# Optimization experiments

Measured on AMD Instinct MI355X. Metric: run time of the kernel, lower is better.

Reference implementation:

```python
import jax, jax.numpy as jnp
import numpy as np

NUM_EMBEDDINGS = 8192
EMBEDDING_DIM = 512
COMMITMENT_COST = 0.25


def setup_inputs() -> dict:
    key = jax.random.key(0)
    kx, ke = jax.random.split(key)
    x = jax.random.normal(kx, (32, 512, 512), dtype=jnp.float32)
    # codebook ~ uniform init as in nn.Embedding default-ish; scale is arbitrary for a reference
    codebook = jax.random.normal(ke, (NUM_EMBEDDINGS, EMBEDDING_DIM), dtype=jnp.float32)
    return {"x": x, "codebook": codebook}


def reference(x, codebook):
    # x: [B, T, D], codebook: [K, D]
    input_shape = x.shape
    flat = x.reshape(-1, EMBEDDING_DIM)                     # [N, D]
    x2 = jnp.sum(flat * flat, axis=1, keepdims=True)        # [N, 1]
    e2 = jnp.sum(codebook * codebook, axis=1)               # [K]
    dists = x2 + e2 - 2.0 * jnp.matmul(flat, codebook.T)    # [N, K]
    encoding_indices = jnp.argmin(dists, axis=1)            # [N] int
    min_distances = jnp.min(dists, axis=1)                  # [N]
    quantized = codebook[encoding_indices].reshape(input_shape)  # [B, T, D]
    # straight-through estimator
    quantized_st = x + jax.lax.stop_gradient(quantized - x)
    # losses (sum reduction, matching F.mse_loss(..., reduction='sum'))
    loss_vq = jnp.sum((quantized - jax.lax.stop_gradient(x)) ** 2)
    loss_commit = jnp.sum((x - jax.lax.stop_gradient(quantized)) ** 2)
    # use_ema = False -> loss includes codebook term
    loss = loss_commit * COMMITMENT_COST + loss_vq
    encoding_indices = encoding_indices.reshape(input_shape[:-1])
    min_distances = min_distances.reshape(input_shape[:-1])
    return quantized_st, loss, encoding_indices, min_distances, loss_commit
```

## Files before the change

### kernel.cpp

```cpp
#include <hip/hip_runtime.h>
#include <hip/hip_bf16.h>
#include <math.h>

#define NUM_EMB 8192
#define DIM 512
#define NROWS 16384
#define NPART 4096

typedef unsigned short ushort;
typedef unsigned long long ull;
typedef __attribute__((ext_vector_type(8))) short short8;
typedef __attribute__((ext_vector_type(4))) float floatx4;

__device__ __forceinline__ ushort f2bf(float f) {
    unsigned u = __float_as_uint(f);
    unsigned r = (u + 0x7fffu + ((u >> 16) & 1u)) >> 16;
    return (ushort)r;
}
__device__ __forceinline__ float bf2f(ushort h) {
    return __uint_as_float(((unsigned)h) << 16);
}
__device__ __forceinline__ unsigned fmap(float f) {
    unsigned u = __float_as_uint(f);
    return (u & 0x80000000u) ? ~u : (u | 0x80000000u);
}
__device__ __forceinline__ float funmap(unsigned m) {
    return __uint_as_float((m & 0x80000000u) ? (m ^ 0x80000000u) : ~m);
}
__device__ __forceinline__ void gld16(const void* g, void* l) {
    __builtin_amdgcn_global_load_lds(
        (const __attribute__((address_space(1))) void*)g,
        (__attribute__((address_space(3))) void*)l, 16, 0, 0);
}

__global__ __launch_bounds__(256) void split_rss_k(const float* __restrict__ src,
    ushort* __restrict__ hi, ushort* __restrict__ lo, float* __restrict__ ss,
    ull* __restrict__ packed, int nrows)
{
    int gid  = blockIdx.x * blockDim.x + threadIdx.x;
    int row  = gid >> 6;
    int lane = threadIdx.x & 63;
    if (row >= nrows) return;
    const float4* r = (const float4*)(src + (size_t)row * DIM);
    ushort4* h4 = (ushort4*)(hi + (size_t)row * DIM);
    ushort4* l4 = (ushort4*)(lo + (size_t)row * DIM);
    float s = 0.f;
#pragma unroll
    for (int i = lane; i < DIM / 4; i += 64) {
        float4 v = r[i];
        s += v.x * v.x + v.y * v.y + v.z * v.z + v.w * v.w;
        ushort4 h, l;
        h.x = f2bf(v.x); l.x = f2bf(v.x - bf2f(h.x));
        h.y = f2bf(v.y); l.y = f2bf(v.y - bf2f(h.y));
        h.z = f2bf(v.z); l.z = f2bf(v.z - bf2f(h.z));
        h.w = f2bf(v.w); l.w = f2bf(v.w - bf2f(h.w));
        h4[i] = h; l4[i] = l;
    }
#pragma unroll
    for (int off = 32; off > 0; off >>= 1) s += __shfl_down(s, off, 64);
    if (lane == 0) {
        ss[row] = s;
        if (packed) packed[row] = ~0ull;
    }
}

__global__ __launch_bounds__(512, 2) void dist_mfma_k(
    const ushort* __restrict__ xh, const ushort* __restrict__ xl,
    const ushort* __restrict__ ch, const ushort* __restrict__ cl,
    const float* __restrict__ e2, ull* __restrict__ packed)
{
    __shared__ ushort Ah[2][256 * 32];
    __shared__ ushort Al[2][256 * 32];
    __shared__ ushort Bh[2][256 * 32];
    __shared__ ushort Bl[2][256 * 32];

    const int tid  = threadIdx.x;
    const int lane = tid & 63;
    const int w    = tid >> 6;
    const int wm   = w >> 2, wn = w & 3;
    const int row0 = blockIdx.x * 256;
    const int col0 = blockIdx.y * 256;

    floatx4 acc[8][4];
#pragma unroll
    for (int m = 0; m < 8; ++m)
#pragma unroll
        for (int n = 0; n < 4; ++n) acc[m][n] = (floatx4){0.f, 0.f, 0.f, 0.f};

    const int c0 = tid, c1 = tid + 512;
    const int r0c = c0 >> 2, s0c = ((c0 & 3) ^ ((c0 >> 3) & 3)) * 8;
    const int r1c = c1 >> 2, s1c = ((c1 & 3) ^ ((c1 >> 3) & 3)) * 8;
    const int ga0 = (row0 + r0c) * DIM + s0c;
    const int ga1 = (row0 + r1c) * DIM + s1c;
    const int gb0 = (col0 + r0c) * DIM + s0c;
    const int gb1 = (col0 + r1c) * DIM + s1c;
    const int l0 = c0 * 8, l1 = c1 * 8;

    const int fr = (lane & 15) * 32 + (((lane >> 4) ^ ((lane >> 1) & 3)) * 8);

    auto stage = [&](int B, int kk) {
        const int dk = kk * 32;
        gld16(&xh[ga0 + dk], &Ah[B][l0]);  gld16(&xh[ga1 + dk], &Ah[B][l1]);
        gld16(&xl[ga0 + dk], &Al[B][l0]);  gld16(&xl[ga1 + dk], &Al[B][l1]);
        gld16(&ch[gb0 + dk], &Bh[B][l0]);  gld16(&ch[gb1 + dk], &Bh[B][l1]);
        gld16(&cl[gb0 + dk], &Bl[B][l0]);  gld16(&cl[gb1 + dk], &Bl[B][l1]);
    };
    auto compute = [&](int B) {
        short8 bh[4], bl[4];
#pragma unroll
        for (int n = 0; n < 4; ++n) {
            const int o = (wn * 64 + n * 16) * 32 + fr;
            bh[n] = *(const short8*)&Bh[B][o];
            bl[n] = *(const short8*)&Bl[B][o];
        }
#pragma unroll
        for (int m = 0; m < 8; ++m) {
            const int o = (wm * 128 + m * 16) * 32 + fr;
            short8 ah = *(const short8*)&Ah[B][o];
            short8 al = *(const short8*)&Al[B][o];
#pragma unroll
            for (int n = 0; n < 4; ++n) {
                acc[m][n] = __builtin_amdgcn_mfma_f32_16x16x32_bf16(ah, bh[n], acc[m][n], 0, 0, 0);
                acc[m][n] = __builtin_amdgcn_mfma_f32_16x16x32_bf16(ah, bl[n], acc[m][n], 0, 0, 0);
                acc[m][n] = __builtin_amdgcn_mfma_f32_16x16x32_bf16(al, bh[n], acc[m][n], 0, 0, 0);
            }
        }
    };

    stage(0, 0);
    __syncthreads();
    int cur = 0;
#pragma unroll 1
    for (int kk = 0; kk < 15; ++kk) {
        stage(cur ^ 1, kk + 1);
        compute(cur);
        __syncthreads();
        cur ^= 1;
    }
    compute(cur);

    float e2v[4];
    int   cidx[4];
#pragma unroll
    for (int n = 0; n < 4; ++n) {
        cidx[n] = col0 + wn * 64 + n * 16 + (lane & 15);
        e2v[n]  = e2[cidx[n]];
    }
#pragma unroll
    for (int m = 0; m < 8; ++m) {
#pragma unroll
        for (int r = 0; r < 4; ++r) {
            float bv = INFINITY; int bi = 0x7fffffff;
#pragma unroll
            for (int n = 0; n < 4; ++n) {
                float v = e2v[n] - 2.f * acc[m][n][r];
                if (v < bv) { bv = v; bi = cidx[n]; }
            }
#pragma unroll
            for (int mk = 1; mk < 16; mk <<= 1) {
                float ov = __shfl_xor(bv, mk, 64);
                int   oi = __shfl_xor(bi, mk, 64);
                if (ov < bv || (ov == bv && oi < bi)) { bv = ov; bi = oi; }
            }
            if ((lane & 15) == 0) {
                int grow = row0 + wm * 128 + m * 16 + (lane >> 4) * 4 + r;
                ull pack = ((ull)fmap(bv) << 32) | (unsigned)bi;
                atomicMin(&packed[grow], pack);
            }
        }
    }
}

__global__ __launch_bounds__(256) void gather_loss_k(const float* __restrict__ x,
    const float* __restrict__ cb, const ull* __restrict__ packed,
    const float* __restrict__ x2, float* __restrict__ outq,
    float* __restrict__ out_idx, float* __restrict__ out_mind,
    float* __restrict__ partials)
{
    __shared__ float ps[4];
    int gid  = blockIdx.x * blockDim.x + threadIdx.x;
    int row  = gid >> 6;
    int lane = threadIdx.x & 63;
    int w    = threadIdx.x >> 6;
    float s = 0.f;
    if (row < NROWS) {
        ull p = packed[row];
        int k = (int)(p & 0xffffffffull);
        if (lane == 0) {
            out_idx[row]  = (float)k;
            out_mind[row] = x2[row] + funmap((unsigned)(p >> 32));
        }
        const float4* q  = (const float4*)(cb + (size_t)k * DIM);
        const float4* xr = (const float4*)(x + (size_t)row * DIM);
        float4* o = (float4*)(outq + (size_t)row * DIM);
#pragma unroll
        for (int i = lane; i < DIM / 4; i += 64) {
            float4 qv = q[i], xv = xr[i];
            o[i] = qv;
            float dx = xv.x - qv.x, dy = xv.y - qv.y;
            float dz = xv.z - qv.z, dw = xv.w - qv.w;
            s += dx * dx + dy * dy + dz * dz + dw * dw;
        }
    }
#pragma unroll
    for (int off = 32; off > 0; off >>= 1) s += __shfl_down(s, off, 64);
    if (lane == 0) ps[w] = s;
    __syncthreads();
    if (threadIdx.x == 0) partials[blockIdx.x] = ps[0] + ps[1] + ps[2] + ps[3];
}

__global__ __launch_bounds__(256) void finalize_k(const float* __restrict__ partials,
    float* __restrict__ out_loss, float* __restrict__ out_commit)
{
    __shared__ float ps[4];
    int t = threadIdx.x, lane = t & 63, w = t >> 6;
    float s = 0.f;
#pragma unroll
    for (int i = 0; i < NPART / 256; ++i) s += partials[t + 256 * i];
#pragma unroll
    for (int off = 32; off > 0; off >>= 1) s += __shfl_down(s, off, 64);
    if (lane == 0) ps[w] = s;
    __syncthreads();
    if (t == 0) {
        float tot = ps[0] + ps[1] + ps[2] + ps[3];
        *out_loss   = 0.25f * tot + tot;
        *out_commit = tot;
    }
}

#define BM 64
#define BN 64
#define BK 32
#define KSPLIT 4
#define KPER (NUM_EMB / KSPLIT)
#define NCT (KPER / BN)

__global__ __launch_bounds__(256) void rowsumsq_k(const float* __restrict__ a,
                                                  float* __restrict__ out, int nrows)
{
    int gid  = blockIdx.x * blockDim.x + threadIdx.x;
    int row  = gid >> 6;
    int lane = threadIdx.x & 63;
    if (row >= nrows) return;
    const float4* r = (const float4*)(a + (size_t)row * DIM);
    float s = 0.f;
#pragma unroll
    for (int i = lane; i < DIM / 4; i += 64) {
        float4 v = r[i];
        s += v.x * v.x + v.y * v.y + v.z * v.z + v.w * v.w;
    }
#pragma unroll
    for (int off = 32; off > 0; off >>= 1) s += __shfl_down(s, off, 64);
    if (lane == 0) out[row] = s;
}

__global__ __launch_bounds__(256) void dist_argmin_old_k(const float* __restrict__ x,
    const float* __restrict__ cb, const float* __restrict__ e2,
    float* __restrict__ part_m, int* __restrict__ part_i)
{
    __shared__ __align__(16) float As[BK][BM + 4];
    __shared__ __align__(16) float Bs[BK][BN + 4];
    __shared__ float redv[BM][16];
    __shared__ int   redi[BM][16];

    const int row0 = blockIdx.x * BM;
    const int ks   = blockIdx.y;
    const int cbeg = ks * KPER;
    const int t    = threadIdx.x;
    const int tx   = t & 15;
    const int ty   = t >> 4;
    const int ld_d = t & 31;
    const int ld_r = t >> 5;

    float minm[4]; int mini[4];
#pragma unroll
    for (int i = 0; i < 4; ++i) { minm[i] = INFINITY; mini[i] = 0; }

    for (int ct = 0; ct < NCT; ++ct) {
        const int c0 = cbeg + ct * BN;
        float acc[4][4];
#pragma unroll
        for (int i = 0; i < 4; ++i)
#pragma unroll
            for (int j = 0; j < 4; ++j) acc[i][j] = 0.f;
        for (int dc = 0; dc < DIM; dc += BK) {
#pragma unroll
            for (int rr = 0; rr < BM; rr += 8)
                As[ld_d][ld_r + rr] = x[(size_t)(row0 + ld_r + rr) * DIM + dc + ld_d];
#pragma unroll
            for (int rr = 0; rr < BN; rr += 8)
                Bs[ld_d][ld_r + rr] = cb[(size_t)(c0 + ld_r + rr) * DIM + dc + ld_d];
            __syncthreads();
#pragma unroll
            for (int d = 0; d < BK; ++d) {
                float4 av = *(const float4*)&As[d][4 * ty];
                float4 bv = *(const float4*)&Bs[d][4 * tx];
                acc[0][0] += av.x * bv.x; acc[0][1] += av.x * bv.y;
                acc[0][2] += av.x * bv.z; acc[0][3] += av.x * bv.w;
                acc[1][0] += av.y * bv.x; acc[1][1] += av.y * bv.y;
                acc[1][2] += av.y * bv.z; acc[1][3] += av.y * bv.w;
                acc[2][0] += av.z * bv.x; acc[2][1] += av.z * bv.y;
                acc[2][2] += av.z * bv.z; acc[2][3] += av.z * bv.w;
                acc[3][0] += av.w * bv.x; acc[3][1] += av.w * bv.y;
                acc[3][2] += av.w * bv.z; acc[3][3] += av.w * bv.w;
            }
            __syncthreads();
        }
#pragma unroll
        for (int j = 0; j < 4; ++j) {
            const int c = c0 + 4 * tx + j;
            const float e = e2[c];
#pragma unroll
            for (int i = 0; i < 4; ++i) {
                float m = e - 2.f * acc[i][j];
                if (m < minm[i]) { minm[i] = m; mini[i] = c; }
            }
        }
    }
#pragma unroll
    for (int i = 0; i < 4; ++i) {
        redv[4 * ty + i][tx] = minm[i];
        redi[4 * ty + i][tx] = mini[i];
    }
    __syncthreads();
    if (t < BM) {
        float bm = INFINITY; int bi = 0;
#pragma unroll
        for (int c = 0; c < 16; ++c) {
            float v = redv[t][c];
            if (v < bm) { bm = v; bi = redi[t][c]; }
        }
        part_m[(size_t)(row0 + t) * KSPLIT + ks] = bm;
        part_i[(size_t)(row0 + t) * KSPLIT + ks] = bi;
    }
}

__global__ __launch_bounds__(256) void merge_pack_k(const float* __restrict__ part_m,
    const int* __restrict__ part_i, ull* __restrict__ packed)
{
    int row = blockIdx.x * blockDim.x + threadIdx.x;
    if (row >= NROWS) return;
    float bm = INFINITY; int bi = 0;
#pragma unroll
    for (int s = 0; s < KSPLIT; ++s) {
        float v = part_m[(size_t)row * KSPLIT + s];
        if (v < bm) { bm = v; bi = part_i[(size_t)row * KSPLIT + s]; }
    }
    packed[row] = ((ull)fmap(bm) << 32) | (unsigned)bi;
}

extern "C" void kernel_launch(void* const* d_in, const int* in_sizes, int n_in,
                              void* d_out, int out_size, void* d_ws, size_t ws_size,
                              hipStream_t stream)
{
    const float* x  = (const float*)d_in[0];
    const float* cb = (const float*)d_in[1];
    float* out = (float*)d_out;

    float* outq       = out;
    float* out_loss   = out + 8388608;
    float* out_idx    = out + 8388609;
    float* out_mind   = out + 8388609 + 16384;
    float* out_commit = out + 8388609 + 2 * 16384;

    char* ws = (char*)d_ws;
    float* e2      = (float*)ws;   ws += NUM_EMB * 4;
    float* x2      = (float*)ws;   ws += NROWS * 4;
    ull*   packed  = (ull*)ws;     ws += NROWS * 8;
    float* partials= (float*)ws;   ws += NPART * 4;
    ushort* xh = (ushort*)ws;      ws += (size_t)NROWS * DIM * 2;
    ushort* xl = (ushort*)ws;      ws += (size_t)NROWS * DIM * 2;
    ushort* ch = (ushort*)ws;      ws += (size_t)NUM_EMB * DIM * 2;
    ushort* cl = (ushort*)ws;      ws += (size_t)NUM_EMB * DIM * 2;
    size_t need_fast = (size_t)(ws - (char*)d_ws);

    if (ws_size >= need_fast) {
        split_rss_k<<<NROWS / 4, 256, 0, stream>>>(x, xh, xl, x2, packed, NROWS);
        split_rss_k<<<NUM_EMB / 4, 256, 0, stream>>>(cb, ch, cl, e2, (ull*)0, NUM_EMB);
        dim3 grid(NROWS / 256, NUM_EMB / 256);
        dist_mfma_k<<<grid, 512, 0, stream>>>(xh, xl, ch, cl, e2, packed);
    } else {
        rowsumsq_k<<<NUM_EMB / 4, 256, 0, stream>>>(cb, e2, NUM_EMB);
        rowsumsq_k<<<NROWS / 4, 256, 0, stream>>>(x, x2, NROWS);
        float* pm = (float*)((char*)d_ws + NUM_EMB * 4 + NROWS * 4 + NROWS * 8 + NPART * 4);
        int*   pi = (int*)(pm + (size_t)NROWS * KSPLIT);
        dim3 grid(NROWS / BM, KSPLIT);
        dist_argmin_old_k<<<grid, 256, 0, stream>>>(x, cb, e2, pm, pi);
        merge_pack_k<<<NROWS / 256, 256, 0, stream>>>(pm, pi, packed);
    }

    gather_loss_k<<<NROWS / 4, 256, 0, stream>>>(x, cb, packed, x2, outq,
                                                 out_idx, out_mind, partials);
    finalize_k<<<1, 256, 0, stream>>>(partials, out_loss, out_commit);
}
```

Baseline: 529.2 us.

## Interleave global prefetch with quarter-tile MFMA phases in distance GEMM

Splits each K-step of the split-bf16 GEMM into four quadrant phases, each loading a slice of A/B fragments from LDS and issuing part of the next tile's async global-to-LDS copies, then running MFMAs under raised wave priority. Explicit vmcnt waits, raw s_barrier and sched_barrier replace the single __syncthreads per iteration. The copy layout is also reorganised so half-tiles can be issued separately. The aim is to overlap memory traffic with matrix math and to shrink register pressure from holding all fragments at once. In exchange the hand-tuned waitcnt counts are fragile, and more barriers per iteration may add synchronisation cost.

```diff
diff --git a/kernel.cpp b/kernel.cpp
--- a/kernel.cpp
+++ b/kernel.cpp
@@ -87,57 +87,98 @@
 #pragma unroll
         for (int n = 0; n < 4; ++n) acc[m][n] = (floatx4){0.f, 0.f, 0.f, 0.f};
 
-    const int c0 = tid, c1 = tid + 512;
-    const int r0c = c0 >> 2, s0c = ((c0 & 3) ^ ((c0 >> 3) & 3)) * 8;
-    const int r1c = c1 >> 2, s1c = ((c1 & 3) ^ ((c1 >> 3) & 3)) * 8;
-    const int ga0 = (row0 + r0c) * DIM + s0c;
-    const int ga1 = (row0 + r1c) * DIM + s1c;
-    const int gb0 = (col0 + r0c) * DIM + s0c;
-    const int gb1 = (col0 + r1c) * DIM + s1c;
-    const int l0 = c0 * 8, l1 = c1 * 8;
+    const int u = tid & 255, b = tid >> 8;
+    const int p = u & 3;
+    const int r_h0 = b * 128 + (u >> 2);
+    const int r_h1 = r_h0 + 64;
+    const int seg0 = (p ^ ((r_h0 >> 1) & 3)) * 8;
+    const int seg1 = (p ^ ((r_h1 >> 1) & 3)) * 8;
+    const int lo_h0 = (r_h0 * 4 + p) * 8;
+    const int lo_h1 = (r_h1 * 4 + p) * 8;
+    const int gA0 = (row0 + r_h0) * DIM + seg0;
+    const int gA1 = (row0 + r_h1) * DIM + seg1;
+    const int gB0 = (col0 + r_h0) * DIM + seg0;
+    const int gB1 = (col0 + r_h1) * DIM + seg1;
 
     const int fr = (lane & 15) * 32 + (((lane >> 4) ^ ((lane >> 1) & 3)) * 8);
 
-    auto stage = [&](int B, int kk) {
-        const int dk = kk * 32;
-        gld16(&xh[ga0 + dk], &Ah[B][l0]);  gld16(&xh[ga1 + dk], &Ah[B][l1]);
-        gld16(&xl[ga0 + dk], &Al[B][l0]);  gld16(&xl[ga1 + dk], &Al[B][l1]);
-        gld16(&ch[gb0 + dk], &Bh[B][l0]);  gld16(&ch[gb1 + dk], &Bh[B][l1]);
-        gld16(&cl[gb0 + dk], &Bl[B][l0]);  gld16(&cl[gb1 + dk], &Bl[B][l1]);
-    };
-    auto compute = [&](int B) {
-        short8 bh[4], bl[4];
-#pragma unroll
-        for (int n = 0; n < 4; ++n) {
-            const int o = (wn * 64 + n * 16) * 32 + fr;
-            bh[n] = *(const short8*)&Bh[B][o];
-            bl[n] = *(const short8*)&Bl[B][o];
-        }
-#pragma unroll
-        for (int m = 0; m < 8; ++m) {
-            const int o = (wm * 128 + m * 16) * 32 + fr;
-            short8 ah = *(const short8*)&Ah[B][o];
-            short8 al = *(const short8*)&Al[B][o];
-#pragma unroll
-            for (int n = 0; n < 4; ++n) {
-                acc[m][n] = __builtin_amdgcn_mfma_f32_16x16x32_bf16(ah, bh[n], acc[m][n], 0, 0, 0);
-                acc[m][n] = __builtin_amdgcn_mfma_f32_16x16x32_bf16(ah, bl[n], acc[m][n], 0, 0, 0);
-                acc[m][n] = __builtin_amdgcn_mfma_f32_16x16x32_bf16(al, bh[n], acc[m][n], 0, 0, 0);
-            }
-        }
-    };
-
-    stage(0, 0);
-    __syncthreads();
-    int cur = 0;
+    short8 ah[4], al[4], bh[4], bl[4];
+
+#define ISSUE_A(B_, h_, dk_) do { \
+    if (h_) { gld16(&xh[gA1 + (dk_)], &Ah[B_][lo_h1]); gld16(&xl[gA1 + (dk_)], &Al[B_][lo_h1]); } \
+    else    { gld16(&xh[gA0 + (dk_)], &Ah[B_][lo_h0]); gld16(&xl[gA0 + (dk_)], &Al[B_][lo_h0]); } } while (0)
+#define ISSUE_B(B_, h_, dk_) do { \
+    if (h_) { gld16(&ch[gB1 + (dk_)], &Bh[B_][lo_h1]); gld16(&cl[gB1 + (dk_)], &Bl[B_][lo_h1]); } \
+    else    { gld16(&ch[gB0 + (dk_)], &Bh[B_][lo_h0]); gld16(&cl[gB0 + (dk_)], &Bl[B_][lo_h0]); } } while (0)
+#define LOAD_A(B_, mh_) do { \
+    _Pragma("unroll") for (int m = 0; m < 4; ++m) { \
+        const int o = (wm * 128 + (mh_) * 64 + m * 16) * 32 + fr; \
+        ah[m] = *(const short8*)&Ah[B_][o]; \
+        al[m] = *(const short8*)&Al[B_][o]; } } while (0)
+#define LOAD_B(B_, nh_) do { \
+    _Pragma("unroll") for (int n = 0; n < 2; ++n) { \
+        const int o = (wn * 64 + (nh_) * 32 + n * 16) * 32 + fr; \
+        bh[(nh_) * 2 + n] = *(const short8*)&Bh[B_][o]; \
+        bl[(nh_) * 2 + n] = *(const short8*)&Bl[B_][o]; } } while (0)
+#define DO_MFMA(mh_, nh_) do { \
+    __builtin_amdgcn_s_setprio(1); \
+    _Pragma("unroll") for (int m = 0; m < 4; ++m) \
+    _Pragma("unroll") for (int n = 0; n < 2; ++n) { \
+        acc[(mh_) * 4 + m][(nh_) * 2 + n] = __builtin_amdgcn_mfma_f32_16x16x32_bf16(ah[m], bh[(nh_) * 2 + n], acc[(mh_) * 4 + m][(nh_) * 2 + n], 0, 0, 0); \
+        acc[(mh_) * 4 + m][(nh_) * 2 + n] = __builtin_amdgcn_mfma_f32_16x16x32_bf16(ah[m], bl[(nh_) * 2 + n], acc[(mh_) * 4 + m][(nh_) * 2 + n], 0, 0, 0); \
+        acc[(mh_) * 4 + m][(nh_) * 2 + n] = __builtin_amdgcn_mfma_f32_16x16x32_bf16(al[m], bh[(nh_) * 2 + n], acc[(mh_) * 4 + m][(nh_) * 2 + n], 0, 0, 0); \
+    } \
+    __builtin_amdgcn_s_setprio(0); } while (0)
+
+    ISSUE_A(0, 0, 0);
+    ISSUE_B(0, 0, 0);
+    ISSUE_B(0, 1, 0);
+    ISSUE_A(0, 1, 0);
+    asm volatile("s_waitcnt vmcnt(0)" ::: "memory");
+    __builtin_amdgcn_s_barrier();
+    __builtin_amdgcn_sched_barrier(0);
+
 #pragma unroll 1
-    for (int kk = 0; kk < 15; ++kk) {
-        stage(cur ^ 1, kk + 1);
-        compute(cur);
-        __syncthreads();
-        cur ^= 1;
-    }
-    compute(cur);
+    for (int t = 0; t < 16; ++t) {
+        const int B = t & 1, Bn = B ^ 1;
+        const int dkn = (t + 1) * 32;
+        const bool pf = (t < 15);
+
+        LOAD_A(B, 0);
+        LOAD_B(B, 0);
+        if (pf) ISSUE_A(Bn, 0, dkn);
+        DO_MFMA(0, 0);
+        if (pf) { asm volatile("s_waitcnt vmcnt(4)" ::: "memory"); }
+        else    { asm volatile("s_waitcnt vmcnt(2)" ::: "memory"); }
+        __builtin_amdgcn_s_barrier();
+        __builtin_amdgcn_sched_barrier(0);
+
+        LOAD_B(B, 1);
+        if (pf) ISSUE_B(Bn, 0, dkn);
+        DO_MFMA(0, 1);
+        if (pf) { asm volatile("s_waitcnt vmcnt(4)" ::: "memory"); }
+        else    { asm volatile("s_waitcnt vmcnt(0)" ::: "memory"); }
+        __builtin_amdgcn_s_barrier();
+        __builtin_amdgcn_sched_barrier(0);
+
+        LOAD_A(B, 1);
+        if (pf) ISSUE_B(Bn, 1, dkn);
+        DO_MFMA(1, 1);
+        __builtin_amdgcn_s_barrier();
+        __builtin_amdgcn_sched_barrier(0);
+
+        if (pf) ISSUE_A(Bn, 1, dkn);
+        DO_MFMA(1, 0);
+        if (pf) { asm volatile("s_waitcnt vmcnt(4)" ::: "memory"); }
+        __builtin_amdgcn_s_barrier();
+        __builtin_amdgcn_sched_barrier(0);
+    }
+
+#undef ISSUE_A
+#undef ISSUE_B
+#undef LOAD_A
+#undef LOAD_B
+#undef DO_MFMA
 
     float e2v[4];
     int   cidx[4];
```

Measured after the change: 512.2 us. 1.03x faster.
